# Kernel optimization log

Hardware: AMD Instinct MI355X
Metric: run time of the kernel (lower is better)

The kernel has to match this reference:

```python
import jax, jax.numpy as jnp
import numpy as np

B, H, S, D = 8, 8, 1024, 64
MAX_REL = 512
VOCAB = 2 * MAX_REL + 1  # 1025


def setup_inputs() -> dict:
    key = jax.random.key(0)
    kq, kk, kv, kwk, kwv = jax.random.split(key, 5)
    q = jax.random.normal(kq, (B, H, S, D), dtype=jnp.float32)
    k = jax.random.normal(kk, (B, H, S, D), dtype=jnp.float32)
    v = jax.random.normal(kv, (B, H, S, D), dtype=jnp.float32)
    W_rel_keys = jax.random.normal(kwk, (VOCAB, D), dtype=jnp.float32) * 0.02
    W_rel_vals = jax.random.normal(kwv, (VOCAB, D), dtype=jnp.float32) * 0.02
    # Clipped relative positions, shifted to [0, 2*MAX_REL]: rel[i, j] = clip(j - i) + MAX_REL
    idx = jnp.arange(S)
    rel_positions = (jnp.clip(idx[None, :] - idx[:, None], -MAX_REL, MAX_REL) + MAX_REL).astype(jnp.int32)
    # Causal mask: True where position should be masked (j > i)
    mask = jnp.triu(jnp.ones((S, S), dtype=bool), k=1)[None, None]  # (1,1,S,S)
    return {"q": q, "k": k, "v": v, "W_rel_keys": W_rel_keys,
            "W_rel_vals": W_rel_vals, "rel_positions": rel_positions, "mask": mask}


def reference(q, k, v, W_rel_keys, W_rel_vals, rel_positions, mask):
    # Embedding lookups: (S, S, D)
    rel_keys = W_rel_keys[rel_positions]
    rel_vals = W_rel_vals[rel_positions]
    # relative_attention(q, k, rel_keys, transpose=True):
    #   q @ k^T  +  per-query-position matmul with rel_keys
    logits = (jnp.einsum('bhid,bhjd->bhij', q, k)
              + jnp.einsum('bhid,ijd->bhij', q, rel_keys))  # (B,H,S,S); NOTE: no 1/sqrt(d) scaling, as in source
    logits = jnp.where(mask, -jnp.inf, logits)
    weights = jax.nn.softmax(logits, axis=-1)
    # dropout p=0.0 (eval) -> identity
    # relative_attention(weights, v, rel_vals, transpose=False)
    output = (jnp.einsum('bhij,bhjd->bhid', weights, v)
              + jnp.einsum('bhij,ijd->bhid', weights, rel_vals))  # (B,H,S,D)
    return (output, weights)
```

## Files before the change

kernel.cpp:

```cpp
#include <hip/hip_runtime.h>
#include <math.h>

#define SS 1024
#define DD 64
#define BH 64

typedef __attribute__((ext_vector_type(4))) float fx4;
typedef __attribute__((ext_vector_type(8))) short sx8;
typedef __attribute__((ext_vector_type(4))) short sx4;

__device__ __forceinline__ unsigned short f2bf(float x) {
  unsigned u = __builtin_bit_cast(unsigned, x);
  u += 0x7fffu + ((u >> 16) & 1u);
  return (unsigned short)(u >> 16);
}
__device__ __forceinline__ float bf2f(unsigned short h) {
  return __builtin_bit_cast(float, ((unsigned)h) << 16);
}

__global__ __launch_bounds__(256, 3) void k_fused(
    const float* __restrict__ q, const float* __restrict__ k,
    const float* __restrict__ v, const float* __restrict__ RK,
    const float* __restrict__ RV, float* __restrict__ W, float* __restrict__ O) {
  const int bid = (blockIdx.y << 3) | blockIdx.x;
  const int nb = ((bid & 7) << 6) | (bid >> 3);
  const int p = nb & 7, bh = nb >> 3;

  __shared__ __align__(16) char smem[54272];
  short* const sKh = (short*)smem;
  short* const sKl = (short*)(smem + 9216);
  short* const sRh = (short*)(smem + 18432);
  short* const vT  = (short*)smem;
  short* const rvT = (short*)(smem + 9472);
  short* const wA  = (short*)(smem + 27136);
  short* const wSk = (short*)(smem + 36864);
  float* const rowInvLds = (float*)(smem + 27136);

  const int t = threadIdx.x;
  const int lane = t & 63, mt = t >> 6, quad = lane >> 4, lc = lane & 15;

#pragma unroll
  for (int e = 0; e < 4; ++e) {
    const int rr = quad * 4 + e;
    const int rloc = mt * 16 + rr;
    const int du = 63 + lc - rr;
    const int us0 = du & 15;
    const int A = (du >> 4) - mt;
#pragma unroll
    for (int kk = 0; kk < 8; ++kk) {
      if (kk < A || kk > A + 3) wSk[rloc * 136 + us0 + 16 * kk] = 0;
    }
  }

  auto stageKRK = [&](const int j0, const int i0) {
    for (int idx = t; idx < 1024; idx += 256) {
      const int row = idx >> 4, c4 = (idx & 15) * 4;
      const float4 x = *(const float4*)(k + ((size_t)(bh * SS + j0 + row)) * DD + c4);
      const float xs[4] = {x.x, x.y, x.z, x.w};
      sx4 h, l;
#pragma unroll
      for (int e = 0; e < 4; ++e) {
        const unsigned short hb = f2bf(xs[e]);
        h[e] = (short)hb;
        l[e] = (short)f2bf(xs[e] - bf2f(hb));
      }
      *(sx4*)&sKh[row * 72 + c4] = h;
      *(sx4*)&sKl[row * 72 + c4] = l;
    }
    const int pLo = j0 - i0 - 63 + 512;
    for (int idx = t; idx < 2048; idx += 256) {
      const int u = idx >> 4, c4 = (idx & 15) * 4;
      int pp = pLo + u;
      pp = pp < 0 ? 0 : (pp > 512 ? 512 : pp);
      const float4 x = *(const float4*)(RK + (size_t)pp * DD + c4);
      sx4 h;
      h[0] = (short)f2bf(x.x); h[1] = (short)f2bf(x.y);
      h[2] = (short)f2bf(x.z); h[3] = (short)f2bf(x.w);
      *(sx4*)&sRh[u * 72 + c4] = h;
    }
  };

  for (int half = 0; half < 2; ++half) {
    const int it = half ? 15 - p : p;
    const int i0 = it << 6;

    {
      const int r = t >> 2, g = t & 3;
      float* Wrow = W + ((size_t)(bh * SS + i0 + r)) * SS;
      float4 z; z.x = z.y = z.z = z.w = 0.f;
      for (int j = (it + 1) * 64 + g * 4; j < SS; j += 16) *(float4*)(Wrow + j) = z;
    }

    sx8 aQh[2], aQl[2];
    {
      const float* qrow = q + ((size_t)(bh * SS + i0 + mt * 16 + lc)) * DD;
#pragma unroll
      for (int ks = 0; ks < 2; ++ks) {
        const int koff = ks * 32 + quad * 8;
        const float4 x0 = *(const float4*)(qrow + koff);
        const float4 x1 = *(const float4*)(qrow + koff + 4);
        const float xs[8] = {x0.x, x0.y, x0.z, x0.w, x1.x, x1.y, x1.z, x1.w};
#pragma unroll
        for (int e = 0; e < 8; ++e) {
          const unsigned short hb = f2bf(xs[e]);
          aQh[ks][e] = (short)hb;
          aQl[ks][e] = (short)f2bf(xs[e] - bf2f(hb));
        }
      }
    }

    const fx4 zz = {0.f, 0.f, 0.f, 0.f};
    float sAcc[4] = {0.f, 0.f, 0.f, 0.f};
    fx4 accO[4] = {zz, zz, zz, zz};

    for (int jt = 0; jt <= it; ++jt) {
      const int j0 = jt * 64;
      const int pLo = j0 - i0 - 63 + 512;
      if (jt | half) __syncthreads();
      stageKRK(j0, i0);
      __syncthreads();

      fx4 accS1[4] = {zz, zz, zz, zz};
      fx4 accS2[5] = {zz, zz, zz, zz, zz};
#pragma unroll
      for (int ks = 0; ks < 2; ++ks) {
        const int koff = ks * 32 + quad * 8;
#pragma unroll
        for (int nt = 0; nt < 4; ++nt) {
          const sx8 bKh = *(const sx8*)&sKh[(nt * 16 + lc) * 72 + koff];
          const sx8 bKl = *(const sx8*)&sKl[(nt * 16 + lc) * 72 + koff];
          accS1[nt] = __builtin_amdgcn_mfma_f32_16x16x32_bf16(aQh[ks], bKh, accS1[nt], 0, 0, 0);
          accS1[nt] = __builtin_amdgcn_mfma_f32_16x16x32_bf16(aQl[ks], bKh, accS1[nt], 0, 0, 0);
          accS1[nt] = __builtin_amdgcn_mfma_f32_16x16x32_bf16(aQh[ks], bKl, accS1[nt], 0, 0, 0);
        }
#pragma unroll
        for (int s = 0; s < 5; ++s) {
          const sx8 bR = *(const sx8*)&sRh[((3 - mt + s) * 16 + lc) * 72 + koff];
          accS2[s] = __builtin_amdgcn_mfma_f32_16x16x32_bf16(aQh[ks], bR, accS2[s], 0, 0, 0);
        }
      }
      __syncthreads();

      for (int idx = t; idx < 1024; idx += 256) {
        const int jj = idx >> 4, d4 = (idx & 15) * 4;
        const float4 x4 = *(const float4*)(v + ((size_t)(bh * SS + j0 + jj)) * DD + d4);
        vT[(d4 + 0) * 74 + jj] = (short)f2bf(x4.x);
        vT[(d4 + 1) * 74 + jj] = (short)f2bf(x4.y);
        vT[(d4 + 2) * 74 + jj] = (short)f2bf(x4.z);
        vT[(d4 + 3) * 74 + jj] = (short)f2bf(x4.w);
      }
      for (int idx = t; idx < 2048; idx += 256) {
        const int u = idx >> 4, d4 = (idx & 15) * 4;
        int pp = pLo + u;
        pp = pp < 0 ? 0 : (pp > 512 ? 512 : pp);
        const float4 x4 = *(const float4*)(RV + (size_t)pp * DD + d4);
        rvT[(d4 + 0) * 138 + u] = (short)f2bf(x4.x);
        rvT[(d4 + 1) * 138 + u] = (short)f2bf(x4.y);
        rvT[(d4 + 2) * 138 + u] = (short)f2bf(x4.z);
        rvT[(d4 + 3) * 138 + u] = (short)f2bf(x4.w);
      }

#pragma unroll
      for (int nt = 0; nt < 4; ++nt) {
#pragma unroll
        for (int e = 0; e < 4; ++e) {
          const int rr = quad * 4 + e;
          const int du = 63 + lc - rr;
          const int srcLane = (lane & 48) | (du & 15);
          const float g0 = __shfl(accS2[nt][e], srcLane, 64);
          const float g1 = __shfl(accS2[nt + 1][e], srcLane, 64);
          const float val = accS1[nt][e] + (du < 64 ? g0 : g1);
          const int col = j0 + nt * 16 + lc;
          const int rowg = i0 + mt * 16 + rr;
          const float w = (col <= rowg) ? __expf(val) : 0.f;
          sAcc[e] += w;
          const unsigned short h = f2bf(w);
          wA[(mt * 16 + rr) * 72 + nt * 16 + lc] = (short)h;
          wSk[(mt * 16 + rr) * 136 + du + 16 * (nt - mt)] = (short)h;
        }
      }
      __syncthreads();

      {
        const int sub = t >> 4;
        const int cq = t & 15;
#pragma unroll
        for (int pass = 0; pass < 4; ++pass) {
          const int row = pass * 16 + sub;
          const sx4 hv = *(const sx4*)&wA[row * 72 + cq * 4];
          float4 o;
          o.x = bf2f((unsigned short)hv[0]);
          o.y = bf2f((unsigned short)hv[1]);
          o.z = bf2f((unsigned short)hv[2]);
          o.w = bf2f((unsigned short)hv[3]);
          *(float4*)(W + ((size_t)(bh * SS + i0 + row)) * SS + j0 + cq * 4) = o;
        }
      }

#pragma unroll
      for (int ks = 0; ks < 2; ++ks) {
        const int koff = ks * 32 + quad * 8;
        const sx8 aW = *(const sx8*)&wA[(mt * 16 + lc) * 72 + koff];
#pragma unroll
        for (int nt = 0; nt < 4; ++nt) {
          const sx8 bV = *(const sx8*)&vT[(nt * 16 + lc) * 74 + koff];
          accO[nt] = __builtin_amdgcn_mfma_f32_16x16x32_bf16(aW, bV, accO[nt], 0, 0, 0);
        }
      }
#pragma unroll
      for (int ks = 0; ks < 4; ++ks) {
        const int koff = ks * 32 + quad * 8;
        const sx8 aS = *(const sx8*)&wSk[(mt * 16 + lc) * 136 + koff];
#pragma unroll
        for (int nt = 0; nt < 4; ++nt) {
          const sx8 bR = *(const sx8*)&rvT[(nt * 16 + lc) * 138 + koff];
          accO[nt] = __builtin_amdgcn_mfma_f32_16x16x32_bf16(aS, bR, accO[nt], 0, 0, 0);
        }
      }
    }

    __syncthreads();

#pragma unroll
    for (int off = 1; off <= 8; off <<= 1) {
#pragma unroll
      for (int e = 0; e < 4; ++e) sAcc[e] += __shfl_xor(sAcc[e], off, 64);
    }
    float rI[4];
#pragma unroll
    for (int e = 0; e < 4; ++e) rI[e] = 1.f / sAcc[e];

    if (lc == 0) {
#pragma unroll
      for (int e = 0; e < 4; ++e) rowInvLds[mt * 16 + quad * 4 + e] = rI[e];
    }

#pragma unroll
    for (int nt = 0; nt < 4; ++nt) {
#pragma unroll
      for (int e = 0; e < 4; ++e) {
        O[((size_t)(bh * SS + i0 + mt * 16 + quad * 4 + e)) * DD + nt * 16 + lc] =
            accO[nt][e] * rI[e];
      }
    }

    __syncthreads();
    __threadfence_block();
    {
      const int r = t >> 2, g = t & 3;
      const float inv = rowInvLds[r];
      float* __restrict__ Wrow = W + ((size_t)(bh * SS + i0 + r)) * SS;
      const int ncol = i0 + 64;
      for (int j = g * 4; j < ncol; j += 16) {
        float4 x = *(const float4*)(Wrow + j);
        x.x *= inv; x.y *= inv; x.z *= inv; x.w *= inv;
        *(float4*)(Wrow + j) = x;
      }
    }
    __syncthreads();
  }
}

extern "C" void kernel_launch(void* const* d_in, const int* in_sizes, int n_in,
                              void* d_out, int out_size, void* d_ws, size_t ws_size,
                              hipStream_t stream) {
  const float* q = (const float*)d_in[0];
  const float* k = (const float*)d_in[1];
  const float* v = (const float*)d_in[2];
  const float* RK = (const float*)d_in[3];
  const float* RV = (const float*)d_in[4];

  float* O = (float*)d_out;
  float* W = (float*)d_out + (size_t)BH * SS * DD;

  k_fused<<<dim3(8, BH), 256, 0, stream>>>(q, k, v, RK, RV, W, O);
}
```

Measured before the change: 624.1 us.

## Split causal row-pairs into separate blocks and register-prefetch next K/RK tile

Measured after the change: 812.4 us. +30.2%, slower.

```diff
diff --git a/kernel.cpp b/kernel.cpp
--- a/kernel.cpp
+++ b/kernel.cpp
@@ -22,9 +22,11 @@
     const float* __restrict__ q, const float* __restrict__ k,
     const float* __restrict__ v, const float* __restrict__ RK,
     const float* __restrict__ RV, float* __restrict__ W, float* __restrict__ O) {
-  const int bid = (blockIdx.y << 3) | blockIdx.x;
-  const int nb = ((bid & 7) << 6) | (bid >> 3);
-  const int p = nb & 7, bh = nb >> 3;
+  const int bid = (blockIdx.y << 4) | blockIdx.x;
+  const int xcd = bid & 7, rest = bid >> 3;
+  const int it = 15 - (rest & 15);
+  const int bh = (xcd << 3) | (rest >> 4);
+  const int i0 = it << 6;
 
   __shared__ __align__(16) char smem[54272];
   short* const sKh = (short*)smem;
@@ -52,11 +54,28 @@
     }
   }
 
-  auto stageKRK = [&](const int j0, const int i0) {
-    for (int idx = t; idx < 1024; idx += 256) {
+  float4 kpf[4], rkpf[8];
+  auto issueKRK = [&](const int j0) {
+#pragma unroll
+    for (int i2 = 0; i2 < 4; ++i2) {
+      const int idx = t + (i2 << 8);
+      kpf[i2] = *(const float4*)(k + ((size_t)(bh * SS + j0 + (idx >> 4))) * DD + (idx & 15) * 4);
+    }
+    const int pLo = j0 - i0 - 63 + 512;
+#pragma unroll
+    for (int i2 = 0; i2 < 8; ++i2) {
+      const int idx = t + (i2 << 8);
+      int pp = pLo + (idx >> 4);
+      pp = pp < 0 ? 0 : (pp > 512 ? 512 : pp);
+      rkpf[i2] = *(const float4*)(RK + (size_t)pp * DD + (idx & 15) * 4);
+    }
+  };
+  auto stageKRKregs = [&]() {
+#pragma unroll
+    for (int i2 = 0; i2 < 4; ++i2) {
+      const int idx = t + (i2 << 8);
       const int row = idx >> 4, c4 = (idx & 15) * 4;
-      const float4 x = *(const float4*)(k + ((size_t)(bh * SS + j0 + row)) * DD + c4);
-      const float xs[4] = {x.x, x.y, x.z, x.w};
+      const float xs[4] = {kpf[i2].x, kpf[i2].y, kpf[i2].z, kpf[i2].w};
       sx4 h, l;
 #pragma unroll
       for (int e = 0; e < 4; ++e) {
@@ -67,197 +86,193 @@
       *(sx4*)&sKh[row * 72 + c4] = h;
       *(sx4*)&sKl[row * 72 + c4] = l;
     }
+#pragma unroll
+    for (int i2 = 0; i2 < 8; ++i2) {
+      const int idx = t + (i2 << 8);
+      const int u = idx >> 4, c4 = (idx & 15) * 4;
+      sx4 h;
+      h[0] = (short)f2bf(rkpf[i2].x); h[1] = (short)f2bf(rkpf[i2].y);
+      h[2] = (short)f2bf(rkpf[i2].z); h[3] = (short)f2bf(rkpf[i2].w);
+      *(sx4*)&sRh[u * 72 + c4] = h;
+    }
+  };
+
+  issueKRK(0);
+
+  {
+    const int r = t >> 2, g = t & 3;
+    float* Wrow = W + ((size_t)(bh * SS + i0 + r)) * SS;
+    float4 z; z.x = z.y = z.z = z.w = 0.f;
+    for (int j = (it + 1) * 64 + g * 4; j < SS; j += 16) *(float4*)(Wrow + j) = z;
+  }
+
+  sx8 aQh[2], aQl[2];
+  {
+    const float* qrow = q + ((size_t)(bh * SS + i0 + mt * 16 + lc)) * DD;
+#pragma unroll
+    for (int ks = 0; ks < 2; ++ks) {
+      const int koff = ks * 32 + quad * 8;
+      const float4 x0 = *(const float4*)(qrow + koff);
+      const float4 x1 = *(const float4*)(qrow + koff + 4);
+      const float xs[8] = {x0.x, x0.y, x0.z, x0.w, x1.x, x1.y, x1.z, x1.w};
+#pragma unroll
+      for (int e = 0; e < 8; ++e) {
+        const unsigned short hb = f2bf(xs[e]);
+        aQh[ks][e] = (short)hb;
+        aQl[ks][e] = (short)f2bf(xs[e] - bf2f(hb));
+      }
+    }
+  }
+
+  const fx4 zz = {0.f, 0.f, 0.f, 0.f};
+  float sAcc[4] = {0.f, 0.f, 0.f, 0.f};
+  fx4 accO[4] = {zz, zz, zz, zz};
+
+  for (int jt = 0; jt <= it; ++jt) {
+    const int j0 = jt * 64;
     const int pLo = j0 - i0 - 63 + 512;
+    if (jt) __syncthreads();
+    stageKRKregs();
+    __syncthreads();
+
+    if (jt < it) issueKRK(j0 + 64);
+
+    fx4 accS1[4] = {zz, zz, zz, zz};
+    fx4 accS2[5] = {zz, zz, zz, zz, zz};
+#pragma unroll
+    for (int ks = 0; ks < 2; ++ks) {
+      const int koff = ks * 32 + quad * 8;
+#pragma unroll
+      for (int nt = 0; nt < 4; ++nt) {
+        const sx8 bKh = *(const sx8*)&sKh[(nt * 16 + lc) * 72 + koff];
+        const sx8 bKl = *(const sx8*)&sKl[(nt * 16 + lc) * 72 + koff];
+        accS1[nt] = __builtin_amdgcn_mfma_f32_16x16x32_bf16(aQh[ks], bKh, accS1[nt], 0, 0, 0);
+        accS1[nt] = __builtin_amdgcn_mfma_f32_16x16x32_bf16(aQl[ks], bKh, accS1[nt], 0, 0, 0);
+        accS1[nt] = __builtin_amdgcn_mfma_f32_16x16x32_bf16(aQh[ks], bKl, accS1[nt], 0, 0, 0);
+      }
+#pragma unroll
+      for (int s = 0; s < 5; ++s) {
+        const sx8 bR = *(const sx8*)&sRh[((3 - mt + s) * 16 + lc) * 72 + koff];
+        accS2[s] = __builtin_amdgcn_mfma_f32_16x16x32_bf16(aQh[ks], bR, accS2[s], 0, 0, 0);
+      }
+    }
+    __syncthreads();
+
+    for (int idx = t; idx < 1024; idx += 256) {
+      const int jj = idx >> 4, d4 = (idx & 15) * 4;
+      const float4 x4 = *(const float4*)(v + ((size_t)(bh * SS + j0 + jj)) * DD + d4);
+      vT[(d4 + 0) * 74 + jj] = (short)f2bf(x4.x);
+      vT[(d4 + 1) * 74 + jj] = (short)f2bf(x4.y);
+      vT[(d4 + 2) * 74 + jj] = (short)f2bf(x4.z);
+      vT[(d4 + 3) * 74 + jj] = (short)f2bf(x4.w);
+    }
     for (int idx = t; idx < 2048; idx += 256) {
-      const int u = idx >> 4, c4 = (idx & 15) * 4;
+      const int u = idx >> 4, d4 = (idx & 15) * 4;
       int pp = pLo + u;
       pp = pp < 0 ? 0 : (pp > 512 ? 512 : pp);
-      const float4 x = *(const float4*)(RK + (size_t)pp * DD + c4);
-      sx4 h;
-      h[0] = (short)f2bf(x.x); h[1] = (short)f2bf(x.y);
-      h[2] = (short)f2bf(x.z); h[3] = (short)f2bf(x.w);
-      *(sx4*)&sRh[u * 72 + c4] = h;
-    }
-  };
-
-  for (int half = 0; half < 2; ++half) {
-    const int it = half ? 15 - p : p;
-    const int i0 = it << 6;
+      const float4 x4 = *(const float4*)(RV + (size_t)pp * DD + d4);
+      rvT[(d4 + 0) * 138 + u] = (short)f2bf(x4.x);
+      rvT[(d4 + 1) * 138 + u] = (short)f2bf(x4.y);
+      rvT[(d4 + 2) * 138 + u] = (short)f2bf(x4.z);
+      rvT[(d4 + 3) * 138 + u] = (short)f2bf(x4.w);
+    }
+
+#pragma unroll
+    for (int nt = 0; nt < 4; ++nt) {
+#pragma unroll
+      for (int e = 0; e < 4; ++e) {
+        const int rr = quad * 4 + e;
+        const int du = 63 + lc - rr;
+        const int srcLane = (lane & 48) | (du & 15);
+        const float g0 = __shfl(accS2[nt][e], srcLane, 64);
+        const float g1 = __shfl(accS2[nt + 1][e], srcLane, 64);
+        const float val = accS1[nt][e] + (du < 64 ? g0 : g1);
+        const int col = j0 + nt * 16 + lc;
+        const int rowg = i0 + mt * 16 + rr;
+        const float w = (col <= rowg) ? __expf(val) : 0.f;
+        sAcc[e] += w;
+        const unsigned short h = f2bf(w);
+        wA[(mt * 16 + rr) * 72 + nt * 16 + lc] = (short)h;
+        wSk[(mt * 16 + rr) * 136 + du + 16 * (nt - mt)] = (short)h;
+      }
+    }
+    __syncthreads();
 
     {
-      const int r = t >> 2, g = t & 3;
-      float* Wrow = W + ((size_t)(bh * SS + i0 + r)) * SS;
-      float4 z; z.x = z.y = z.z = z.w = 0.f;
-      for (int j = (it + 1) * 64 + g * 4; j < SS; j += 16) *(float4*)(Wrow + j) = z;
-    }
-
-    sx8 aQh[2], aQl[2];
-    {
-      const float* qrow = q + ((size_t)(bh * SS + i0 + mt * 16 + lc)) * DD;
-#pragma unroll
-      for (int ks = 0; ks < 2; ++ks) {
-        const int koff = ks * 32 + quad * 8;
-        const float4 x0 = *(const float4*)(qrow + koff);
-        const float4 x1 = *(const float4*)(qrow + koff + 4);
-        const float xs[8] = {x0.x, x0.y, x0.z, x0.w, x1.x, x1.y, x1.z, x1.w};
-#pragma unroll
-        for (int e = 0; e < 8; ++e) {
-          const unsigned short hb = f2bf(xs[e]);
-          aQh[ks][e] = (short)hb;
-          aQl[ks][e] = (short)f2bf(xs[e] - bf2f(hb));
-        }
-      }
-    }
-
-    const fx4 zz = {0.f, 0.f, 0.f, 0.f};
-    float sAcc[4] = {0.f, 0.f, 0.f, 0.f};
-    fx4 accO[4] = {zz, zz, zz, zz};
-
-    for (int jt = 0; jt <= it; ++jt) {
-      const int j0 = jt * 64;
-      const int pLo = j0 - i0 - 63 + 512;
-      if (jt | half) __syncthreads();
-      stageKRK(j0, i0);
-      __syncthreads();
-
-      fx4 accS1[4] = {zz, zz, zz, zz};
-      fx4 accS2[5] = {zz, zz, zz, zz, zz};
-#pragma unroll
-      for (int ks = 0; ks < 2; ++ks) {
-        const int koff = ks * 32 + quad * 8;
-#pragma unroll
-        for (int nt = 0; nt < 4; ++nt) {
-          const sx8 bKh = *(const sx8*)&sKh[(nt * 16 + lc) * 72 + koff];
-          const sx8 bKl = *(const sx8*)&sKl[(nt * 16 + lc) * 72 + koff];
-          accS1[nt] = __builtin_amdgcn_mfma_f32_16x16x32_bf16(aQh[ks], bKh, accS1[nt], 0, 0, 0);
-          accS1[nt] = __builtin_amdgcn_mfma_f32_16x16x32_bf16(aQl[ks], bKh, accS1[nt], 0, 0, 0);
-          accS1[nt] = __builtin_amdgcn_mfma_f32_16x16x32_bf16(aQh[ks], bKl, accS1[nt], 0, 0, 0);
-        }
-#pragma unroll
-        for (int s = 0; s < 5; ++s) {
-          const sx8 bR = *(const sx8*)&sRh[((3 - mt + s) * 16 + lc) * 72 + koff];
-          accS2[s] = __builtin_amdgcn_mfma_f32_16x16x32_bf16(aQh[ks], bR, accS2[s], 0, 0, 0);
-        }
-      }
-      __syncthreads();
-
-      for (int idx = t; idx < 1024; idx += 256) {
-        const int jj = idx >> 4, d4 = (idx & 15) * 4;
-        const float4 x4 = *(const float4*)(v + ((size_t)(bh * SS + j0 + jj)) * DD + d4);
-        vT[(d4 + 0) * 74 + jj] = (short)f2bf(x4.x);
-        vT[(d4 + 1) * 74 + jj] = (short)f2bf(x4.y);
-        vT[(d4 + 2) * 74 + jj] = (short)f2bf(x4.z);
-        vT[(d4 + 3) * 74 + jj] = (short)f2bf(x4.w);
-      }
-      for (int idx = t; idx < 2048; idx += 256) {
-        const int u = idx >> 4, d4 = (idx & 15) * 4;
-        int pp = pLo + u;
-        pp = pp < 0 ? 0 : (pp > 512 ? 512 : pp);
-        const float4 x4 = *(const float4*)(RV + (size_t)pp * DD + d4);
-        rvT[(d4 + 0) * 138 + u] = (short)f2bf(x4.x);
-        rvT[(d4 + 1) * 138 + u] = (short)f2bf(x4.y);
-        rvT[(d4 + 2) * 138 + u] = (short)f2bf(x4.z);
-        rvT[(d4 + 3) * 138 + u] = (short)f2bf(x4.w);
-      }
-
+      const int sub = t >> 4;
+      const int cq = t & 15;
+#pragma unroll
+      for (int pass = 0; pass < 4; ++pass) {
+        const int row = pass * 16 + sub;
+        const sx4 hv = *(const sx4*)&wA[row * 72 + cq * 4];
+        float4 o;
+        o.x = bf2f((unsigned short)hv[0]);
+        o.y = bf2f((unsigned short)hv[1]);
+        o.z = bf2f((unsigned short)hv[2]);
+        o.w = bf2f((unsigned short)hv[3]);
+        *(float4*)(W + ((size_t)(bh * SS + i0 + row)) * SS + j0 + cq * 4) = o;
+      }
+    }
+
+#pragma unroll
+    for (int ks = 0; ks < 2; ++ks) {
+      const int koff = ks * 32 + quad * 8;
+      const sx8 aW = *(const sx8*)&wA[(mt * 16 + lc) * 72 + koff];
 #pragma unroll
       for (int nt = 0; nt < 4; ++nt) {
-#pragma unroll
-        for (int e = 0; e < 4; ++e) {
-          const int rr = quad * 4 + e;
-          const int du = 63 + lc - rr;
-          const int srcLane = (lane & 48) | (du & 15);
-          const float g0 = __shfl(accS2[nt][e], srcLane, 64);
-          const float g1 = __shfl(accS2[nt + 1][e], srcLane, 64);
-          const float val = accS1[nt][e] + (du < 64 ? g0 : g1);
-          const int col = j0 + nt * 16 + lc;
-          const int rowg = i0 + mt * 16 + rr;
-          const float w = (col <= rowg) ? __expf(val) : 0.f;
-          sAcc[e] += w;
-          const unsigned short h = f2bf(w);
-          wA[(mt * 16 + rr) * 72 + nt * 16 + lc] = (short)h;
-          wSk[(mt * 16 + rr) * 136 + du + 16 * (nt - mt)] = (short)h;
-        }
-      }
-      __syncthreads();
-
-      {
-        const int sub = t >> 4;
-        const int cq = t & 15;
-#pragma unroll
-        for (int pass = 0; pass < 4; ++pass) {
-          const int row = pass * 16 + sub;
-          const sx4 hv = *(const sx4*)&wA[row * 72 + cq * 4];
-          float4 o;
-          o.x = bf2f((unsigned short)hv[0]);
-          o.y = bf2f((unsigned short)hv[1]);
-          o.z = bf2f((unsigned short)hv[2]);
-          o.w = bf2f((unsigned short)hv[3]);
-          *(float4*)(W + ((size_t)(bh * SS + i0 + row)) * SS + j0 + cq * 4) = o;
-        }
-      }
-
-#pragma unroll
-      for (int ks = 0; ks < 2; ++ks) {
-        const int koff = ks * 32 + quad * 8;
-        const sx8 aW = *(const sx8*)&wA[(mt * 16 + lc) * 72 + koff];
-#pragma unroll
-        for (int nt = 0; nt < 4; ++nt) {
-          const sx8 bV = *(const sx8*)&vT[(nt * 16 + lc) * 74 + koff];
-          accO[nt] = __builtin_amdgcn_mfma_f32_16x16x32_bf16(aW, bV, accO[nt], 0, 0, 0);
-        }
-      }
-#pragma unroll
-      for (int ks = 0; ks < 4; ++ks) {
-        const int koff = ks * 32 + quad * 8;
-        const sx8 aS = *(const sx8*)&wSk[(mt * 16 + lc) * 136 + koff];
-#pragma unroll
-        for (int nt = 0; nt < 4; ++nt) {
-          const sx8 bR = *(const sx8*)&rvT[(nt * 16 + lc) * 138 + koff];
-          accO[nt] = __builtin_amdgcn_mfma_f32_16x16x32_bf16(aS, bR, accO[nt], 0, 0, 0);
-        }
-      }
-    }
-
-    __syncthreads();
-
-#pragma unroll
-    for (int off = 1; off <= 8; off <<= 1) {
-#pragma unroll
-      for (int e = 0; e < 4; ++e) sAcc[e] += __shfl_xor(sAcc[e], off, 64);
-    }
-    float rI[4];
-#pragma unroll
-    for (int e = 0; e < 4; ++e) rI[e] = 1.f / sAcc[e];
-
-    if (lc == 0) {
-#pragma unroll
-      for (int e = 0; e < 4; ++e) rowInvLds[mt * 16 + quad * 4 + e] = rI[e];
-    }
-
-#pragma unroll
-    for (int nt = 0; nt < 4; ++nt) {
-#pragma unroll
-      for (int e = 0; e < 4; ++e) {
-        O[((size_t)(bh * SS + i0 + mt * 16 + quad * 4 + e)) * DD + nt * 16 + lc] =
-            accO[nt][e] * rI[e];
-      }
-    }
-
-    __syncthreads();
-    __threadfence_block();
-    {
-      const int r = t >> 2, g = t & 3;
-      const float inv = rowInvLds[r];
-      float* __restrict__ Wrow = W + ((size_t)(bh * SS + i0 + r)) * SS;
-      const int ncol = i0 + 64;
-      for (int j = g * 4; j < ncol; j += 16) {
-        float4 x = *(const float4*)(Wrow + j);
-        x.x *= inv; x.y *= inv; x.z *= inv; x.w *= inv;
-        *(float4*)(Wrow + j) = x;
-      }
-    }
-    __syncthreads();
+        const sx8 bV = *(const sx8*)&vT[(nt * 16 + lc) * 74 + koff];
+        accO[nt] = __builtin_amdgcn_mfma_f32_16x16x32_bf16(aW, bV, accO[nt], 0, 0, 0);
+      }
+    }
+#pragma unroll
+    for (int ks = 0; ks < 4; ++ks) {
+      const int koff = ks * 32 + quad * 8;
+      const sx8 aS = *(const sx8*)&wSk[(mt * 16 + lc) * 136 + koff];
+#pragma unroll
+      for (int nt = 0; nt < 4; ++nt) {
+        const sx8 bR = *(const sx8*)&rvT[(nt * 16 + lc) * 138 + koff];
+        accO[nt] = __builtin_amdgcn_mfma_f32_16x16x32_bf16(aS, bR, accO[nt], 0, 0, 0);
+      }
+    }
+  }
+
+  __syncthreads();
+
+#pragma unroll
+  for (int off = 1; off <= 8; off <<= 1) {
+#pragma unroll
+    for (int e = 0; e < 4; ++e) sAcc[e] += __shfl_xor(sAcc[e], off, 64);
+  }
+  float rI[4];
+#pragma unroll
+  for (int e = 0; e < 4; ++e) rI[e] = 1.f / sAcc[e];
+
+  if (lc == 0) {
+#pragma unroll
+    for (int e = 0; e < 4; ++e) rowInvLds[mt * 16 + quad * 4 + e] = rI[e];
+  }
+
+#pragma unroll
+  for (int nt = 0; nt < 4; ++nt) {
+#pragma unroll
+    for (int e = 0; e < 4; ++e) {
+      O[((size_t)(bh * SS + i0 + mt * 16 + quad * 4 + e)) * DD + nt * 16 + lc] =
+          accO[nt][e] * rI[e];
+    }
+  }
+
+  __syncthreads();
+  __threadfence_block();
+  {
+    const int r = t >> 2, g = t & 3;
+    const float inv = rowInvLds[r];
+    float* __restrict__ Wrow = W + ((size_t)(bh * SS + i0 + r)) * SS;
+    const int ncol = i0 + 64;
+    for (int j = g * 4; j < ncol; j += 16) {
+      float4 x = *(const float4*)(Wrow + j);
+      x.x *= inv; x.y *= inv; x.z *= inv; x.w *= inv;
+      *(float4*)(Wrow + j) = x;
+    }
   }
 }
 
@@ -273,5 +288,5 @@
   float* O = (float*)d_out;
   float* W = (float*)d_out + (size_t)BH * SS * DD;
 
-  k_fused<<<dim3(8, BH), 256, 0, stream>>>(q, k, v, RK, RV, W, O);
-}
+  k_fused<<<dim3(16, BH), 256, 0, stream>>>(q, k, v, RK, RV, W, O);
+}
```
